# Kernel optimization log

Hardware: AMD Instinct MI355X
Metric: run time of the kernel (lower is better)

Reference implementation:

```python
import jax, jax.numpy as jnp
import numpy as np

DIM = 1024
HEADS = 16
DIM_HEAD = 64
SCALE = DIM_HEAD ** -0.5
LN_EPS = 1e-5


def layer_norm(x, g, b):
    mu = jnp.mean(x, axis=-1, keepdims=True)
    var = jnp.mean(jnp.square(x - mu), axis=-1, keepdims=True)
    return (x - mu) * jax.lax.rsqrt(var + LN_EPS) * g + b


def setup_inputs() -> dict:
    key = jax.random.key(0)
    ks = jax.random.split(key, 8)
    w_std = DIM ** -0.5  # keep GEMM outputs O(1)
    return {
        "query": jax.random.normal(ks[0], (4, 512, DIM), jnp.float32),
        "kv": jax.random.normal(ks[1], (4, 2048, DIM), jnp.float32),
        "ln_q_g": jnp.ones((DIM,), jnp.float32),
        "ln_q_b": jnp.zeros((DIM,), jnp.float32),
        "ln_kv_g": jnp.ones((DIM,), jnp.float32),
        "ln_kv_b": jnp.zeros((DIM,), jnp.float32),
        "Wq": jax.random.normal(ks[2], (DIM, DIM), jnp.float32) * w_std,
        "bq": jnp.zeros((DIM,), jnp.float32),
        "Wk": jax.random.normal(ks[3], (DIM, DIM), jnp.float32) * w_std,
        "bk": jnp.zeros((DIM,), jnp.float32),
        "Wv": jax.random.normal(ks[4], (DIM, DIM), jnp.float32) * w_std,
        "bv": jnp.zeros((DIM,), jnp.float32),
        "Wo": jax.random.normal(ks[5], (DIM, DIM), jnp.float32) * w_std,
        "bo": jnp.zeros((DIM,), jnp.float32),
    }


def reference(query, kv, ln_q_g, ln_q_b, ln_kv_g, ln_kv_b,
              Wq, bq, Wk, bk, Wv, bv, Wo, bo):
    kv_n = layer_norm(kv, ln_kv_g, ln_kv_b)            # (b, n_kv, d)
    residual = query
    q_n = layer_norm(query, ln_q_g, ln_q_b)            # (b, n_q, d)

    q = q_n @ Wq + bq                                   # (b, n_q, inner)
    kv_input = jnp.concatenate((kv_n, q_n), axis=-2)    # (b, n_kv+n_q, d)
    k = kv_input @ Wk + bk
    v = kv_input @ Wv + bv

    def split_heads(t):
        b, n, _ = t.shape
        return t.reshape(b, n, HEADS, DIM_HEAD).transpose(0, 2, 1, 3)  # b h n dh

    q = split_heads(q) * SCALE
    k = split_heads(k)
    v = split_heads(v)

    sim = jnp.einsum('bhid,bhjd->bhij', q, k)           # (b, h, n_q, n_kv+n_q)
    sim = sim - jax.lax.stop_gradient(jnp.max(sim, axis=-1, keepdims=True))
    attn = jax.nn.softmax(sim, axis=-1)
    out = jnp.einsum('bhij,bhjd->bhid', attn, v)        # (b, h, n_q, dh)

    b, h, n, dh = out.shape
    out = out.transpose(0, 2, 1, 3).reshape(b, n, h * dh)
    return out @ Wo + bo + residual
```

## Files before the change

kernel.cpp:

```cpp
#include <hip/hip_runtime.h>
#include <hip/hip_bf16.h>

#define B_    4
#define NQ    512
#define NKV   2048
#define NT    2560
#define DIM_  1024
#define HEADS 16
#define DH    64
#define NSEQT 10240
#define SCALE_Q_L2E 0.18033688011112042f

typedef short bf16x8 __attribute__((ext_vector_type(8)));
typedef float f32x4  __attribute__((ext_vector_type(4)));
typedef __hip_bfloat16 bf16;

__device__ inline void gll16(const bf16* g, bf16* l) {
  __builtin_amdgcn_global_load_lds(
      (const __attribute__((address_space(1))) unsigned int*)g,
      (__attribute__((address_space(3))) unsigned int*)l, 16, 0, 0);
}

__global__ __launch_bounds__(256) void prep_kernel(
    const float* __restrict__ query, const float* __restrict__ kv,
    const float* __restrict__ lgq, const float* __restrict__ lbq,
    const float* __restrict__ lgkv, const float* __restrict__ lbkv,
    bf16* __restrict__ X,
    const float* __restrict__ W0, const float* __restrict__ W1,
    const float* __restrict__ W2, const float* __restrict__ W3,
    bf16* __restrict__ T0, bf16* __restrict__ T1,
    bf16* __restrict__ T2, bf16* __restrict__ T3)
{
  __shared__ __align__(16) char psm[9216];
  const int t = threadIdx.x;
  const int blkid = blockIdx.x;
  if (blkid < B_*NT) {
    float* sh = (float*)psm;
    int b = blkid / NT, r = blkid % NT;
    const float *src, *g, *bb;
    if (r < NKV) { src = kv    + ((size_t)b*NKV + r)*DIM_;      g = lgkv; bb = lbkv; }
    else         { src = query + ((size_t)b*NQ + (r-NKV))*DIM_; g = lgq;  bb = lbq;  }
    float4 v = ((const float4*)src)[t];
    float s  = v.x+v.y+v.z+v.w;
    float s2 = v.x*v.x+v.y*v.y+v.z*v.z+v.w*v.w;
    #pragma unroll
    for (int m=1;m<64;m<<=1){ s += __shfl_xor(s,m,64); s2 += __shfl_xor(s2,m,64); }
    int wave=t>>6, lane=t&63;
    if(lane==0){ sh[wave]=s; sh[4+wave]=s2; }
    __syncthreads();
    s  = sh[0]+sh[1]+sh[2]+sh[3];
    s2 = sh[4]+sh[5]+sh[6]+sh[7];
    float mu = s*(1.0f/DIM_);
    float rs = rsqrtf(s2*(1.0f/DIM_) - mu*mu + 1e-5f);
    float4 gg = ((const float4*)g)[t];
    float4 b4 = ((const float4*)bb)[t];
    bf16* dst = X + (size_t)blkid*DIM_ + t*4;
    dst[0]=__float2bfloat16((v.x-mu)*rs*gg.x + b4.x);
    dst[1]=__float2bfloat16((v.y-mu)*rs*gg.y + b4.y);
    dst[2]=__float2bfloat16((v.z-mu)*rs*gg.z + b4.z);
    dst[3]=__float2bfloat16((v.w-mu)*rs*gg.w + b4.w);
  } else {
    int l = blkid - B_*NT;
    const float* W; bf16* Wt;
    switch (l>>8) {
      case 0: W=W0; Wt=T0; break;
      case 1: W=W1; Wt=T1; break;
      case 2: W=W2; Wt=T2; break;
      default: W=W3; Wt=T3; break;
    }
    int rem = l & 255;
    int k0 = (rem&15)*64, n0 = (rem>>4)*64;
    bf16* Ws = (bf16*)psm;
    int kr = t>>2, nseg = (t&3)*16;
    const float4* s4 = (const float4*)(W + (size_t)(k0+kr)*DIM_ + n0 + nseg);
    union { uint4 u[2]; bf16 h[16]; } pk;
    #pragma unroll
    for (int j=0;j<4;j++){
      float4 v = s4[j];
      pk.h[j*4+0]=__float2bfloat16(v.x); pk.h[j*4+1]=__float2bfloat16(v.y);
      pk.h[j*4+2]=__float2bfloat16(v.z); pk.h[j*4+3]=__float2bfloat16(v.w);
    }
    *(uint4*)(Ws + kr*72 + nseg)     = pk.u[0];
    *(uint4*)(Ws + kr*72 + nseg + 8) = pk.u[1];
    __syncthreads();
    int n = t&63, kseg = t>>6;
    union { uint4 u[2]; bf16 h[16]; } o;
    #pragma unroll
    for (int k=0;k<16;k++) o.h[k] = Ws[(kseg*16+k)*72 + n];
    bf16* dst = Wt + (size_t)(n0+n)*DIM_ + k0 + kseg*16;
    *(uint4*)dst = o.u[0];
    *(uint4*)(dst+8) = o.u[1];
  }
}

__device__ __forceinline__ void gemm_core(
    const bf16* __restrict__ A, const bf16* __restrict__ Bmat,
    const float* __restrict__ bias, const float* __restrict__ residual,
    void* __restrict__ outv, int rows_per_batch, int row_offset,
    int a_batch_stride_rows, int n_seq, float scale,
    int emode, int m0, int n0, char* smem)
{
  bf16* As = (bf16*)smem;
  bf16* Bs = (bf16*)(smem + 8192);
  float* Ts = (float*)smem;

  const int t = threadIdx.x;
  const int r0 = t>>2, c8 = (t&3)*8;
  int gm0 = m0 + r0, gm1 = m0 + 64 + r0;
  int b0i = gm0 / rows_per_batch, b1i = gm1 / rows_per_batch;
  const bf16* a0 = A + ((size_t)b0i*a_batch_stride_rows + row_offset + (gm0 - b0i*rows_per_batch))*(size_t)DIM_ + c8;
  const bf16* a1 = A + ((size_t)b1i*a_batch_stride_rows + row_offset + (gm1 - b1i*rows_per_batch))*(size_t)DIM_ + c8;
  const bf16* wb0 = Bmat + (size_t)(n0 + r0)*DIM_ + c8;
  const bf16* wb1 = Bmat + (size_t)(n0 + 64 + r0)*DIM_ + c8;
  bf16* lA0 = As + t*8;  bf16* lA1 = As + 64*32 + t*8;
  bf16* lB0 = Bs + t*8;  bf16* lB1 = Bs + 64*32 + t*8;

  const int wave = t>>6, lane = t&63, qq = lane>>4, mr = lane&15;
  const int wm = (wave>>1)*64, wn = (wave&1)*64;

  f32x4 acc[4][4] = {};
  for (int k0 = 0; k0 < DIM_; k0 += 32) {
    gll16(a0 + k0, lA0);
    gll16(a1 + k0, lA1);
    gll16(wb0 + k0, lB0);
    gll16(wb1 + k0, lB1);
    __syncthreads();
    bf16x8 af[4], bfr[4];
    #pragma unroll
    for (int ms=0;ms<4;ms++) af[ms]  = *(const bf16x8*)(As + (wm+ms*16+mr)*32 + qq*8);
    #pragma unroll
    for (int ns=0;ns<4;ns++) bfr[ns] = *(const bf16x8*)(Bs + (wn+ns*16+mr)*32 + qq*8);
    #pragma unroll
    for (int ms=0;ms<4;ms++)
      #pragma unroll
      for (int ns=0;ns<4;ns++)
        acc[ms][ns] = __builtin_amdgcn_mfma_f32_16x16x32_bf16(af[ms], bfr[ns], acc[ms][ns], 0,0,0);
    __syncthreads();
  }

  const int lr = t>>3, cs = (t&7)*16;
  for (int R=0; R<4; R++){
    if ((wave>>1) == (R>>1)) {
      #pragma unroll
      for (int ms2=0; ms2<2; ms2++){
        int ms = (R&1)*2 + ms2;
        #pragma unroll
        for (int ns=0; ns<4; ns++){
          int col = wn + ns*16 + mr;
          #pragma unroll
          for (int r=0;r<4;r++)
            Ts[(ms2*16 + qq*4 + r)*132 + col] = acc[ms][ns][r];
        }
      }
    }
    __syncthreads();
    float v[16];
    #pragma unroll
    for (int j=0;j<4;j++){
      float4 f = *(const float4*)(Ts + lr*132 + cs + j*4);
      v[j*4+0]=f.x; v[j*4+1]=f.y; v[j*4+2]=f.z; v[j*4+3]=f.w;
    }
    int gr = m0 + R*32 + lr;
    int gc = n0 + cs;
    if (emode == 0) {
      float* out = (float*)outv;
      size_t base = (size_t)gr*DIM_ + gc;
      #pragma unroll
      for (int j=0;j<4;j++){
        float4 bv = *(const float4*)(bias + gc + j*4);
        float4 rv = *(const float4*)(residual + base + j*4);
        float4 o4;
        o4.x = v[j*4+0] + bv.x + rv.x;
        o4.y = v[j*4+1] + bv.y + rv.y;
        o4.z = v[j*4+2] + bv.z + rv.z;
        o4.w = v[j*4+3] + bv.w + rv.w;
        *(float4*)(out + base + j*4) = o4;
      }
    } else if (emode == 1) {
      int bb = gr / rows_per_batch;
      int n  = gr - bb*rows_per_batch;
      int hh = gc>>6, dh = gc&63;
      bf16* out = (bf16*)outv + ((size_t)(bb*HEADS + hh)*n_seq + n)*DH + dh;
      union { uint4 u[2]; bf16 h[16]; } pk;
      #pragma unroll
      for (int j=0;j<16;j++) pk.h[j] = __float2bfloat16((v[j] + bias[gc+j])*scale);
      *(uint4*)out     = pk.u[0];
      *(uint4*)(out+8) = pk.u[1];
    } else {
      float bc = bias[gr];
      bf16* out = (bf16*)outv + (size_t)gr*NSEQT + gc;
      union { uint4 u[2]; bf16 h[16]; } pk;
      #pragma unroll
      for (int j=0;j<16;j++) pk.h[j] = __float2bfloat16(v[j] + bc);
      *(uint4*)out     = pk.u[0];
      *(uint4*)(out+8) = pk.u[1];
    }
    __syncthreads();
  }
}

__global__ __launch_bounds__(256) void gemm_qkv(
    const bf16* __restrict__ X,
    const bf16* __restrict__ WtQ, const bf16* __restrict__ WtK,
    const bf16* __restrict__ WtV,
    const float* __restrict__ bq, const float* __restrict__ bk,
    const float* __restrict__ bv,
    bf16* __restrict__ Qhb, bf16* __restrict__ Khb, bf16* __restrict__ VTg)
{
  __shared__ __align__(16) char smem[16896];
  const int blk = blockIdx.x;
  if (blk < 128) {
    gemm_core(X, WtQ, bq, nullptr, Qhb, NQ, NKV, NT, NQ, SCALE_Q_L2E, 1,
              (blk&15)*128, (blk>>4)*128, smem);
  } else if (blk < 768) {
    int l = blk - 128;
    gemm_core(X, WtK, bk, nullptr, Khb, NT, 0, NT, NT, 1.0f, 1,
              (l%80)*128, (l/80)*128, smem);
  } else {
    int l = blk - 768;
    gemm_core(WtV, X, bv, nullptr, VTg, DIM_, 0, DIM_, NSEQT, 1.0f, 2,
              (l&7)*128, (l>>3)*128, smem);
  }
}

__global__ __launch_bounds__(256) void gemm_o(
    const bf16* __restrict__ Ctx, const bf16* __restrict__ WtO,
    const float* __restrict__ bo, const float* __restrict__ residual,
    float* __restrict__ out)
{
  __shared__ __align__(16) char smem[16896];
  const int blk = blockIdx.x;
  gemm_core(Ctx, WtO, bo, residual, out, B_*NQ, 0, B_*NQ, NQ, 1.0f, 0,
            (blk&15)*128, (blk>>4)*128, smem);
}

__global__ __launch_bounds__(256) void attn5_kernel(
    const bf16* __restrict__ Qh, const bf16* __restrict__ Kh,
    const bf16* __restrict__ VTg, bf16* __restrict__ Ctx)
{
  __shared__ __align__(16) bf16 KV[2][8192];
  __shared__ __align__(16) unsigned int Ps[4][576];

  const int t = threadIdx.x, wave = t>>6, lane = t&63;
  const int qq = lane>>4, mr = lane&15;
  const int blk = blockIdx.x;
  const int bh = (blk&7)*8 + (blk>>6);
  const int q0 = ((blk>>3)&7)*64;
  const int b = bh>>4, h = bh&15;

  const int sl = t>>2, sc = t&3;
  const int skey = ((sl&15)<<2) | (sl>>4);
  const bf16* Kb  = Kh + (size_t)bh*NT*DH + (size_t)skey*DH + sc*8;
  const bf16* VbT = VTg + ((size_t)(h*DH) + sl)*NSEQT + (size_t)b*NT + sc*8;

  const bf16* Qb = Qh + ((size_t)bh*NQ + q0 + wave*16 + mr)*DH;
  bf16x8 qf0 = *(const bf16x8*)(Qb + qq*8);
  bf16x8 qf1 = *(const bf16x8*)(Qb + 32 + qq*8);

  f32x4 o[4] = {};
  float l[4] = {};
  unsigned int* Pw = &Ps[wave][0];

  {
    bf16* bp = &KV[0][0];
    gll16(Kb,            bp + t*8);
    gll16(Kb + 32,       bp + 2048 + t*8);
    gll16(VbT,           bp + 4096 + t*8);
    gll16(VbT + 32,      bp + 6144 + t*8);
  }

  for (int it = 0; it < NT/64; it++) {
    __syncthreads();
    if (it + 1 < NT/64) {
      int kt = (it+1)*64;
      bf16* bp = &KV[(it+1)&1][0];
      gll16(Kb  + (size_t)kt*DH, bp + t*8);
      gll16(Kb  + (size_t)kt*DH + 32, bp + 2048 + t*8);
      gll16(VbT + kt,      bp + 4096 + t*8);
      gll16(VbT + kt + 32, bp + 6144 + t*8);
    }
    const bf16* cbuf = &KV[it&1][0];

    bf16x8 kl[4], kh_[4];
    #pragma unroll
    for (int g=0; g<4; g++){
      kl[g]  = *(const bf16x8*)(cbuf + ((g*16+mr)*32 + qq*8));
      kh_[g] = *(const bf16x8*)(cbuf + 2048 + ((g*16+mr)*32 + qq*8));
    }
    f32x4 s[4];
    #pragma unroll
    for (int g=0; g<4; g++){
      f32x4 z = {};
      z = __builtin_amdgcn_mfma_f32_16x16x32_bf16(qf0, kl[g],  z, 0,0,0);
      z = __builtin_amdgcn_mfma_f32_16x16x32_bf16(qf1, kh_[g], z, 0,0,0);
      s[g] = z;
    }
    bf16x8 vl[4], vh[4];
    #pragma unroll
    for (int n2=0; n2<4; n2++){
      vl[n2] = *(const bf16x8*)(cbuf + 4096 + ((n2*16+mr)*32 + qq*8));
      vh[n2] = *(const bf16x8*)(cbuf + 6144 + ((n2*16+mr)*32 + qq*8));
    }
    #pragma unroll
    for (int r=0; r<4; r++){
      float e0 = __builtin_amdgcn_exp2f(s[0][r]);
      float e1 = __builtin_amdgcn_exp2f(s[1][r]);
      float e2 = __builtin_amdgcn_exp2f(s[2][r]);
      float e3 = __builtin_amdgcn_exp2f(s[3][r]);
      l[r] += (e0+e1)+(e2+e3);
      unsigned a0 = __float_as_uint(e0) + 0x8000u;
      unsigned a1 = __float_as_uint(e1) + 0x8000u;
      unsigned a2 = __float_as_uint(e2) + 0x8000u;
      unsigned a3 = __float_as_uint(e3) + 0x8000u;
      uint2 w;
      w.x = __builtin_amdgcn_perm(a1, a0, 0x07060302u);
      w.y = __builtin_amdgcn_perm(a3, a2, 0x07060302u);
      *(uint2*)(Pw + (qq*4+r)*36 + mr*2) = w;
    }
    asm volatile("s_waitcnt lgkmcnt(0)" ::: "memory");
    bf16x8 plo = *(const bf16x8*)(Pw + mr*36 + qq*4);
    bf16x8 phi = *(const bf16x8*)(Pw + mr*36 + qq*4 + 16);
    #pragma unroll
    for (int n2=0; n2<4; n2++){
      o[n2] = __builtin_amdgcn_mfma_f32_16x16x32_bf16(plo, vl[n2], o[n2], 0,0,0);
      o[n2] = __builtin_amdgcn_mfma_f32_16x16x32_bf16(phi, vh[n2], o[n2], 0,0,0);
    }
  }

  float rl[4];
  #pragma unroll
  for (int r=0; r<4; r++){
    float v = l[r];
    #pragma unroll
    for (int m=1;m<16;m<<=1) v += __shfl_xor(v, m, 16);
    rl[r] = 1.0f / v;
  }

  __syncthreads();
  float* OfW = (float*)(&KV[0][0]) + wave*1088;
  #pragma unroll
  for (int n2=0; n2<4; n2++)
    #pragma unroll
    for (int r=0; r<4; r++)
      OfW[(qq*4+r)*68 + n2*16 + mr] = o[n2][r]*rl[r];
  asm volatile("s_waitcnt lgkmcnt(0)" ::: "memory");
  {
    int row = lane>>2, seg = (lane&3)*16;
    union { uint4 u[2]; bf16 hh[16]; } pkv;
    #pragma unroll
    for (int j=0;j<16;j++) pkv.hh[j] = __float2bfloat16(OfW[row*68 + seg + j]);
    bf16* dst = Ctx + ((size_t)b*NQ + q0 + wave*16 + row)*DIM_ + h*DH + seg;
    *(uint4*)dst = pkv.u[0];
    *(uint4*)(dst+8) = pkv.u[1];
  }
}

extern "C" void kernel_launch(void* const* d_in, const int* in_sizes, int n_in,
                              void* d_out, int out_size, void* d_ws, size_t ws_size,
                              hipStream_t stream)
{
  const float* query  = (const float*)d_in[0];
  const float* kv     = (const float*)d_in[1];
  const float* ln_q_g = (const float*)d_in[2];
  const float* ln_q_b = (const float*)d_in[3];
  const float* ln_kv_g= (const float*)d_in[4];
  const float* ln_kv_b= (const float*)d_in[5];
  const float* Wq = (const float*)d_in[6];
  const float* bq = (const float*)d_in[7];
  const float* Wk = (const float*)d_in[8];
  const float* bk = (const float*)d_in[9];
  const float* Wv = (const float*)d_in[10];
  const float* bv = (const float*)d_in[11];
  const float* Wo = (const float*)d_in[12];
  const float* bo = (const float*)d_in[13];
  float* out = (float*)d_out;

  char* ws = (char*)d_ws;
  size_t off = 0;
  auto take = [&](size_t bytes)->char* {
    char* p = ws + off; off += (bytes + 255) & ~(size_t)255; return p;
  };
  bf16* X    = (bf16*)take((size_t)B_*NT*DIM_*2);
  bf16* Qhb  = (bf16*)take((size_t)B_*NQ*DIM_*2);
  bf16* Khb  = (bf16*)take((size_t)B_*NT*DIM_*2);
  bf16* VTg  = (bf16*)take((size_t)DIM_*NSEQT*2);
  bf16* Ctx  = (bf16*)take((size_t)B_*NQ*DIM_*2);
  bf16* WtQ  = (bf16*)take((size_t)DIM_*DIM_*2);
  bf16* WtK  = (bf16*)take((size_t)DIM_*DIM_*2);
  bf16* WtV  = (bf16*)take((size_t)DIM_*DIM_*2);
  bf16* WtO  = (bf16*)take((size_t)DIM_*DIM_*2);

  prep_kernel<<<B_*NT + 1024, 256, 0, stream>>>(
      query, kv, ln_q_g, ln_q_b, ln_kv_g, ln_kv_b, X,
      Wq, Wk, Wv, Wo, WtQ, WtK, WtV, WtO);

  gemm_qkv<<<1408, 256, 0, stream>>>(X, WtQ, WtK, WtV, bq, bk, bv,
                                     Qhb, Khb, VTg);

  attn5_kernel<<<512, 256, 0, stream>>>(Qhb, Khb, VTg, Ctx);

  gemm_o<<<128, 256, 0, stream>>>(Ctx, WtO, bo, query, out);
}
```

Before: 271.9 us.

## Split attention key tile across wave pairs with 32-row query tiles, reorder V GEMM blocks

The attention kernel now gives each pair of waves 32 query rows, and the two waves in a pair each take half of every 64-key tile. Each wave loads half as many K and V fragments from LDS per MFMA, so LDS fragment traffic per unit of work is lower. The two halves' partial outputs and row sums are merged through shared memory at the end, which adds extra barriers and an LDS reduction. The V-projection GEMM block index mapping is also swapped so neighbouring blocks walk along the sequence dimension, which changes the order in which tiles are visited and how they reuse cache.

```diff
diff --git a/kernel.cpp b/kernel.cpp
--- a/kernel.cpp
+++ b/kernel.cpp
@@ -219,7 +219,7 @@
   } else {
     int l = blk - 768;
     gemm_core(WtV, X, bv, nullptr, VTg, DIM_, 0, DIM_, NSEQT, 1.0f, 2,
-              (l&7)*128, (l>>3)*128, smem);
+              (l/80)*128, (l%80)*128, smem);
   }
 }
 
@@ -234,12 +234,12 @@
             (blk&15)*128, (blk>>4)*128, smem);
 }
 
-__global__ __launch_bounds__(256) void attn5_kernel(
+__global__ __launch_bounds__(256) void attn6_kernel(
     const bf16* __restrict__ Qh, const bf16* __restrict__ Kh,
     const bf16* __restrict__ VTg, bf16* __restrict__ Ctx)
 {
   __shared__ __align__(16) bf16 KV[2][8192];
-  __shared__ __align__(16) unsigned int Ps[4][576];
+  __shared__ __align__(16) unsigned int Ps[4][640];
 
   const int t = threadIdx.x, wave = t>>6, lane = t&63;
   const int qq = lane>>4, mr = lane&15;
@@ -247,26 +247,32 @@
   const int bh = (blk&7)*8 + (blk>>6);
   const int q0 = ((blk>>3)&7)*64;
   const int b = bh>>4, h = bh&15;
+  const int pair = wave>>1, kh = wave&1;
+  const int qb = pair*32;
 
   const int sl = t>>2, sc = t&3;
-  const int skey = ((sl&15)<<2) | (sl>>4);
+  const int skey = 32*(sl>>5) + 2*(sl&15) + ((sl>>4)&1);
   const bf16* Kb  = Kh + (size_t)bh*NT*DH + (size_t)skey*DH + sc*8;
   const bf16* VbT = VTg + ((size_t)(h*DH) + sl)*NSEQT + (size_t)b*NT + sc*8;
 
-  const bf16* Qb = Qh + ((size_t)bh*NQ + q0 + wave*16 + mr)*DH;
-  bf16x8 qf0 = *(const bf16x8*)(Qb + qq*8);
-  bf16x8 qf1 = *(const bf16x8*)(Qb + 32 + qq*8);
-
-  f32x4 o[4] = {};
-  float l[4] = {};
+  bf16x8 qf[2][2];
+  #pragma unroll
+  for (int mt=0; mt<2; mt++){
+    const bf16* Qb = Qh + ((size_t)bh*NQ + q0 + qb + mt*16 + mr)*DH;
+    qf[mt][0] = *(const bf16x8*)(Qb + qq*8);
+    qf[mt][1] = *(const bf16x8*)(Qb + 32 + qq*8);
+  }
+
+  f32x4 o[2][4] = {};
+  float l[2][4] = {};
   unsigned int* Pw = &Ps[wave][0];
 
   {
     bf16* bp = &KV[0][0];
-    gll16(Kb,            bp + t*8);
-    gll16(Kb + 32,       bp + 2048 + t*8);
-    gll16(VbT,           bp + 4096 + t*8);
-    gll16(VbT + 32,      bp + 6144 + t*8);
+    gll16(Kb,        bp + t*8);
+    gll16(Kb + 32,   bp + 2048 + t*8);
+    gll16(VbT,       bp + 4096 + t*8);
+    gll16(VbT + 32,  bp + 6144 + t*8);
   }
 
   for (int it = 0; it < NT/64; it++) {
@@ -274,82 +280,107 @@
     if (it + 1 < NT/64) {
       int kt = (it+1)*64;
       bf16* bp = &KV[(it+1)&1][0];
-      gll16(Kb  + (size_t)kt*DH, bp + t*8);
+      gll16(Kb  + (size_t)kt*DH,      bp + t*8);
       gll16(Kb  + (size_t)kt*DH + 32, bp + 2048 + t*8);
-      gll16(VbT + kt,      bp + 4096 + t*8);
-      gll16(VbT + kt + 32, bp + 6144 + t*8);
+      gll16(VbT + kt,                 bp + 4096 + t*8);
+      gll16(VbT + kt + 32,            bp + 6144 + t*8);
     }
     const bf16* cbuf = &KV[it&1][0];
 
-    bf16x8 kl[4], kh_[4];
-    #pragma unroll
-    for (int g=0; g<4; g++){
-      kl[g]  = *(const bf16x8*)(cbuf + ((g*16+mr)*32 + qq*8));
-      kh_[g] = *(const bf16x8*)(cbuf + 2048 + ((g*16+mr)*32 + qq*8));
-    }
-    f32x4 s[4];
-    #pragma unroll
-    for (int g=0; g<4; g++){
-      f32x4 z = {};
-      z = __builtin_amdgcn_mfma_f32_16x16x32_bf16(qf0, kl[g],  z, 0,0,0);
-      z = __builtin_amdgcn_mfma_f32_16x16x32_bf16(qf1, kh_[g], z, 0,0,0);
-      s[g] = z;
-    }
-    bf16x8 vl[4], vh[4];
-    #pragma unroll
-    for (int n2=0; n2<4; n2++){
-      vl[n2] = *(const bf16x8*)(cbuf + 4096 + ((n2*16+mr)*32 + qq*8));
-      vh[n2] = *(const bf16x8*)(cbuf + 6144 + ((n2*16+mr)*32 + qq*8));
-    }
+    bf16x8 kf[2][2];
+    #pragma unroll
+    for (int g=0; g<2; g++){
+      kf[g][0] = *(const bf16x8*)(cbuf + (32*kh + 16*g + mr)*32 + qq*8);
+      kf[g][1] = *(const bf16x8*)(cbuf + 2048 + (32*kh + 16*g + mr)*32 + qq*8);
+    }
+    f32x4 s[2][2];
+    #pragma unroll
+    for (int mt=0; mt<2; mt++)
+      #pragma unroll
+      for (int g=0; g<2; g++){
+        f32x4 z = {};
+        z = __builtin_amdgcn_mfma_f32_16x16x32_bf16(qf[mt][0], kf[g][0], z, 0,0,0);
+        z = __builtin_amdgcn_mfma_f32_16x16x32_bf16(qf[mt][1], kf[g][1], z, 0,0,0);
+        s[mt][g] = z;
+      }
+    bf16x8 vf[4];
+    #pragma unroll
+    for (int n2=0; n2<4; n2++)
+      vf[n2] = *(const bf16x8*)(cbuf + 4096 + kh*2048 + (n2*16+mr)*32 + qq*8);
+
+    #pragma unroll
+    for (int mt=0; mt<2; mt++)
+      #pragma unroll
+      for (int r=0; r<4; r++){
+        float e0 = __builtin_amdgcn_exp2f(s[mt][0][r]);
+        float e1 = __builtin_amdgcn_exp2f(s[mt][1][r]);
+        l[mt][r] += e0 + e1;
+        unsigned a0 = __float_as_uint(e0) + 0x8000u;
+        unsigned a1 = __float_as_uint(e1) + 0x8000u;
+        Pw[(mt*16 + qq*4 + r)*20 + mr] = __builtin_amdgcn_perm(a1, a0, 0x07060302u);
+      }
+    asm volatile("s_waitcnt lgkmcnt(0)" ::: "memory");
+    bf16x8 pa[2];
+    #pragma unroll
+    for (int mt=0; mt<2; mt++)
+      pa[mt] = *(const bf16x8*)(Pw + (mt*16+mr)*20 + qq*4);
+    #pragma unroll
+    for (int mt=0; mt<2; mt++)
+      #pragma unroll
+      for (int n2=0; n2<4; n2++)
+        o[mt][n2] = __builtin_amdgcn_mfma_f32_16x16x32_bf16(pa[mt], vf[n2], o[mt][n2], 0,0,0);
+  }
+
+  float lsum[2][4];
+  #pragma unroll
+  for (int mt=0; mt<2; mt++)
     #pragma unroll
     for (int r=0; r<4; r++){
-      float e0 = __builtin_amdgcn_exp2f(s[0][r]);
-      float e1 = __builtin_amdgcn_exp2f(s[1][r]);
-      float e2 = __builtin_amdgcn_exp2f(s[2][r]);
-      float e3 = __builtin_amdgcn_exp2f(s[3][r]);
-      l[r] += (e0+e1)+(e2+e3);
-      unsigned a0 = __float_as_uint(e0) + 0x8000u;
-      unsigned a1 = __float_as_uint(e1) + 0x8000u;
-      unsigned a2 = __float_as_uint(e2) + 0x8000u;
-      unsigned a3 = __float_as_uint(e3) + 0x8000u;
-      uint2 w;
-      w.x = __builtin_amdgcn_perm(a1, a0, 0x07060302u);
-      w.y = __builtin_amdgcn_perm(a3, a2, 0x07060302u);
-      *(uint2*)(Pw + (qq*4+r)*36 + mr*2) = w;
-    }
-    asm volatile("s_waitcnt lgkmcnt(0)" ::: "memory");
-    bf16x8 plo = *(const bf16x8*)(Pw + mr*36 + qq*4);
-    bf16x8 phi = *(const bf16x8*)(Pw + mr*36 + qq*4 + 16);
-    #pragma unroll
-    for (int n2=0; n2<4; n2++){
-      o[n2] = __builtin_amdgcn_mfma_f32_16x16x32_bf16(plo, vl[n2], o[n2], 0,0,0);
-      o[n2] = __builtin_amdgcn_mfma_f32_16x16x32_bf16(phi, vh[n2], o[n2], 0,0,0);
-    }
-  }
-
-  float rl[4];
-  #pragma unroll
-  for (int r=0; r<4; r++){
-    float v = l[r];
-    #pragma unroll
-    for (int m=1;m<16;m<<=1) v += __shfl_xor(v, m, 16);
-    rl[r] = 1.0f / v;
-  }
+      float v = l[mt][r];
+      #pragma unroll
+      for (int m=1;m<16;m<<=1) v += __shfl_xor(v, m, 16);
+      lsum[mt][r] = v;
+    }
 
   __syncthreads();
-  float* OfW = (float*)(&KV[0][0]) + wave*1088;
-  #pragma unroll
-  for (int n2=0; n2<4; n2++)
-    #pragma unroll
-    for (int r=0; r<4; r++)
-      OfW[(qq*4+r)*68 + n2*16 + mr] = o[n2][r]*rl[r];
-  asm volatile("s_waitcnt lgkmcnt(0)" ::: "memory");
+  float* Of  = (float*)&KV[0][0];
+  float* lsh = (float*)&Ps[0][0];
+  if (kh == 1) {
+    #pragma unroll
+    for (int mt=0; mt<2; mt++){
+      #pragma unroll
+      for (int n2=0; n2<4; n2++)
+        #pragma unroll
+        for (int r=0; r<4; r++)
+          Of[(qb + mt*16 + qq*4 + r)*68 + n2*16 + mr] = o[mt][n2][r];
+      if (mr == 0)
+        #pragma unroll
+        for (int r=0; r<4; r++)
+          lsh[qb + mt*16 + qq*4 + r] = lsum[mt][r];
+    }
+  }
+  __syncthreads();
+  if (kh == 0) {
+    #pragma unroll
+    for (int mt=0; mt<2; mt++)
+      #pragma unroll
+      for (int r=0; r<4; r++){
+        int row = qb + mt*16 + qq*4 + r;
+        float rl = 1.0f / (lsum[mt][r] + lsh[row]);
+        #pragma unroll
+        for (int n2=0; n2<4; n2++){
+          int idx = row*68 + n2*16 + mr;
+          Of[idx] = (o[mt][n2][r] + Of[idx]) * rl;
+        }
+      }
+  }
+  __syncthreads();
   {
-    int row = lane>>2, seg = (lane&3)*16;
+    int row = t>>2, seg = (t&3)*16;
     union { uint4 u[2]; bf16 hh[16]; } pkv;
     #pragma unroll
-    for (int j=0;j<16;j++) pkv.hh[j] = __float2bfloat16(OfW[row*68 + seg + j]);
-    bf16* dst = Ctx + ((size_t)b*NQ + q0 + wave*16 + row)*DIM_ + h*DH + seg;
+    for (int j=0;j<16;j++) pkv.hh[j] = __float2bfloat16(Of[row*68 + seg + j]);
+    bf16* dst = Ctx + ((size_t)b*NQ + q0 + row)*DIM_ + h*DH + seg;
     *(uint4*)dst = pkv.u[0];
     *(uint4*)(dst+8) = pkv.u[1];
   }
@@ -397,7 +428,7 @@
   gemm_qkv<<<1408, 256, 0, stream>>>(X, WtQ, WtK, WtV, bq, bk, bv,
                                      Qhb, Khb, VTg);
 
-  attn5_kernel<<<512, 256, 0, stream>>>(Qhb, Khb, VTg, Ctx);
+  attn6_kernel<<<512, 256, 0, stream>>>(Qhb, Khb, VTg, Ctx);
 
   gemm_o<<<128, 256, 0, stream>>>(Ctx, WtO, bo, query, out);
 }
```

Result: no change. 268.1 us (-1.4%).
